# Kernel optimization log

Hardware: AMD Instinct MI355X
Metric: run time of the kernel (lower is better)

Reference implementation:

```python
import jax, jax.numpy as jnp
import numpy as np
from jax import lax

EPS = 1e-6
PPU = 256        # points_per_unit
MULT = 8         # 2 ** rho.num_halving_layers
C = 3            # in_channels (data channels)
NBASIS = 5
NS = 4           # num_samples
RHO_IN = 16      # encoder out / rho in channels
RHO_OUT = 32     # rho out channels
KW = 5           # conv kernel width


def setup_inputs() -> dict:
    key = jax.random.key(0)
    ks = jax.random.split(key, 16)
    nb, npts, ntar = 16, 2048, 256
    x = jax.random.uniform(ks[0], (nb, npts, C), jnp.float32)
    y = jax.random.normal(ks[1], (nb, npts, C), jnp.float32)
    x_out = jax.random.uniform(ks[2], (nb, ntar, C), jnp.float32)
    # --- compute_xgrid (done concretely at setup; mirrors torch logic) ---
    x_min = float(min(np.min(np.asarray(x)), np.min(np.asarray(x_out)))) - 0.1
    x_max = float(max(np.max(np.asarray(x)), np.max(np.asarray(x_out)))) + 0.1
    ngrid = int(np.ceil(PPU * (x_max - x_min) / MULT) * MULT)  # to_multiple
    grid = jnp.linspace(x_min, x_max, ngrid, dtype=jnp.float32)
    x_grid = jnp.broadcast_to(grid[None, :, None], (nb, ngrid, C))
    # --- parameters ---
    init_l = 2.0 / PPU
    enc_sigma = jnp.log(1e-6 + init_l * jnp.ones((C,), jnp.float32))
    int_sigma = jnp.log(1e-6 + init_l * jnp.ones((NBASIS, C), jnp.float32))
    s = 0.05
    gW = s * jax.random.normal(ks[3], (2 * C, RHO_IN), jnp.float32)
    gb = jnp.zeros((RHO_IN,), jnp.float32)
    w1 = s * jax.random.normal(ks[4], (RHO_OUT, RHO_IN, KW), jnp.float32)
    b1 = jnp.zeros((RHO_OUT,), jnp.float32)
    w2 = s * jax.random.normal(ks[5], (RHO_OUT, RHO_OUT, KW), jnp.float32)
    b2 = jnp.zeros((RHO_OUT,), jnp.float32)
    w3 = s * jax.random.normal(ks[6], (RHO_OUT, RHO_OUT, KW), jnp.float32)
    b3 = jnp.zeros((RHO_OUT,), jnp.float32)
    linW = s * jax.random.normal(ks[7], (RHO_OUT, 2 * C * NBASIS), jnp.float32)
    linb = jnp.zeros((2 * C * NBASIS,), jnp.float32)
    loW = s * jax.random.normal(ks[8], (C * NBASIS, 2 * C), jnp.float32)
    lob = jnp.zeros((2 * C,), jnp.float32)
    eps_noise = jax.random.normal(ks[9], (NS, nb, C * NBASIS), jnp.float32)
    return dict(x=x, y=y, x_out=x_out, x_grid=x_grid, eps_noise=eps_noise,
                enc_sigma=enc_sigma, gW=gW, gb=gb, w1=w1, b1=b1, w2=w2, b2=b2,
                w3=w3, b3=b3, linW=linW, linb=linb, int_sigma=int_sigma,
                loW=loW, lob=lob)


def _conv1d(h, w, b):
    # h: (N, Cin, L), w: (Cout, Cin, K) -> (N, Cout, L)
    return lax.conv_general_dilated(h, w, (1,), 'SAME',
                                    dimension_numbers=('NCH', 'OIH', 'NCH')) + b[None, :, None]


def reference(x, y, x_out, x_grid, eps_noise, enc_sigma, gW, gb,
              w1, b1, w2, b2, w3, b3, linW, linb, int_sigma, loW, lob):
    nb = x.shape[0]
    # ---- ConvDeepSet encoder: context points -> grid ----
    scales = jnp.exp(enc_sigma)                                  # (C,)
    d = (x[:, :, None, :] - x_grid[:, None, :, :]) / (scales + EPS)  # (nb,n,m,C)
    wt = jnp.exp(-0.5 * d * d)
    h0 = wt.sum(axis=1)                                          # (nb,m,C)
    h1 = (y[:, :, None, :] * wt).sum(axis=1)                     # (nb,m,C)
    n_h1 = h1 / (h0 + EPS)
    rep = jnp.concatenate([h0, n_h1], axis=-1) @ gW + gb         # (nb,m,RHO_IN)
    # ---- rho CNN on grid ----
    h = jax.nn.sigmoid(rep).transpose(0, 2, 1)                   # (nb,RHO_IN,m)
    h = jax.nn.relu(_conv1d(h, w1, b1))
    h = jax.nn.relu(_conv1d(h, w2, b2))
    h = _conv1d(h, w3, b3)                                       # (nb,RHO_OUT,m)
    h_grid = h.transpose(0, 2, 1) @ linW + linb                  # (nb,m,2*C*NBASIS)
    h_mu, h_std = jnp.split(h_grid, 2, axis=-1)
    h_std = 0.1 + 0.9 * jax.nn.sigmoid(h_std)
    # ---- latent samples ----
    z = h_mu[None] + h_std[None] * eps_noise[:, :, None, :]      # (NS,nb,m,C*NBASIS)
    ngrid = z.shape[2]
    z = z.reshape(NS * nb, ngrid, NBASIS, C)
    # ---- FinalLayer interpolator: grid -> targets ----
    xg = jnp.broadcast_to(x_grid[None], (NS,) + x_grid.shape).reshape(NS * nb, ngrid, C)
    xt = jnp.broadcast_to(x_out[None], (NS,) + x_out.shape).reshape(NS * nb, -1, C)
    iscales = jnp.exp(int_sigma)                                  # (NBASIS,C)
    dd = (xg[:, :, None, None, :] - xt[:, None, :, None, :]) / (iscales + EPS)
    wtt = jnp.exp(-0.5 * dd * dd)                                 # (NSnb,m,t,NBASIS,C)
    h_out = (z[:, :, None, :, :] * wtt).sum(axis=1)               # (NSnb,t,NBASIS,C)
    ntar = h_out.shape[1]
    out = h_out.reshape(NS * nb, ntar, NBASIS * C) @ loW + lob    # (NSnb,t,2C)
    mu, std = jnp.split(out, 2, axis=-1)
    std = jax.nn.softplus(std)
    return jnp.concatenate([mu, std], axis=-1).reshape(NS, nb, ntar, 2 * C)
```

## Files before the change

### kernel.cpp

```cpp
#include <hip/hip_runtime.h>
#include <math.h>

#define EPSF 1e-6f
#define LOG2E 1.4426950408889634f

__device__ __forceinline__ float sigmoidf_(float v) { return 1.0f / (1.0f + __expf(-v)); }

__global__ __launch_bounds__(512, 1) void encrho_kernel(
    const float* __restrict__ x, const float* __restrict__ y,
    const float* __restrict__ xg, const float* __restrict__ enc_sigma,
    const float* __restrict__ gW, const float* __restrict__ gb,
    const float* __restrict__ w1, const float* __restrict__ b1,
    const float* __restrict__ w2, const float* __restrict__ b2,
    const float* __restrict__ w3, const float* __restrict__ b3,
    const float* __restrict__ linW, const float* __restrict__ linb,
    float* __restrict__ mu, float* __restrict__ stdv,
    int nb, int M)
{
    __shared__ __align__(16) float smem[14856];
    float* sWA = smem;
    float* sWB = smem + 5152;
    float* sH1 = smem + 10304;
    float* sH2 = smem + 11200;
    float* sH3 = smem + 11968;
    float* sIn = smem + 12608;
    float* flt = smem;
    float* red = smem + 13120;
    float* tot = smem + 14656;
    float* sRange = smem + 14848;
    __shared__ int scnt[3];
    __shared__ int spad[3];

    const int tid = threadIdx.x;
    const int b = blockIdx.y;
    const int c0 = blockIdx.x * 20;
    const int ic = tid & 31, ng = tid >> 5;

    {
        float sg0 = __expf(enc_sigma[0]) + EPSF;
        float sg1 = __expf(enc_sigma[1]) + EPSF;
        float sg2 = __expf(enc_sigma[2]) + EPSF;
        float e20 = -0.5f * LOG2E / (sg0 * sg0);
        float e21 = -0.5f * LOG2E / (sg1 * sg1);
        float e22 = -0.5f * LOG2E / (sg2 * sg2);

        int mg = c0 - 6 + ic;
        bool cv = (mg >= 0 && mg < M);
        float g0 = 0, g1 = 0, g2 = 0;
        if (cv) {
            const float* gp = xg + (size_t)(b * M + mg) * 3;
            g0 = gp[0]; g1 = gp[1]; g2 = gp[2];
        }
        if (tid < 3) scnt[tid] = 0;
        if (tid < 96) {
            int c = tid >> 5;
            int col = c0 - 6 + ic;
            col = col < 0 ? 0 : (col >= M ? M - 1 : col);
            float gv = xg[(size_t)(b * M + col) * 3 + c];
            float gmn = gv, gmx = gv;
            #pragma unroll
            for (int mask = 1; mask <= 16; mask <<= 1) {
                gmn = fminf(gmn, __shfl_xor(gmn, mask, 64));
                gmx = fmaxf(gmx, __shfl_xor(gmx, mask, 64));
            }
            if (ic == 0) {
                float sgc = __expf(enc_sigma[c]) + EPSF;
                sRange[c] = gmn - 10.0f * sgc;
                sRange[3 + c] = gmx + 10.0f * sgc;
            }
        }
        __syncthreads();
        {
            const float* xb = x + (size_t)b * 6144;
            const float* yb = y + (size_t)b * 6144;
            #pragma unroll 1
            for (int idx = tid; idx < 6144; idx += 512) {
                float xv = xb[idx];
                int c = idx % 3;
                if (xv >= sRange[c] && xv <= sRange[3 + c]) {
                    int p = atomicAdd(&scnt[c], 1);
                    int o = (c << 12) + (p << 1);
                    flt[o] = xv;
                    flt[o + 1] = yb[idx];
                }
            }
        }
        __syncthreads();
        if (tid < 3) spad[tid] = (scnt[tid] + 31) & ~31;
        __syncthreads();
        #pragma unroll
        for (int c = 0; c < 3; c++) {
            int cnt = scnt[c], cp = spad[c];
            for (int p = cnt + tid; p < cp; p += 512) {
                int o = (c << 12) + (p << 1);
                flt[o] = 1e30f;
                flt[o + 1] = 0.0f;
            }
        }
        __syncthreads();
        float h[6];
        {
            const float2* f = (const float2*)flt;
            int cp = spad[0];
            float s0a = 0, s0b = 0, s1a = 0, s1b = 0;
            #pragma unroll 2
            for (int n = ng; n < cp; n += 32) {
                float2 va = f[n], vb = f[n + 16];
                float da = va.x - g0; float wa = exp2f(e20 * da * da);
                float db = vb.x - g0; float wb = exp2f(e20 * db * db);
                s0a += wa; s1a = fmaf(va.y, wa, s1a);
                s0b += wb; s1b = fmaf(vb.y, wb, s1b);
            }
            h[0] = s0a + s0b; h[3] = s1a + s1b;
        }
        {
            const float2* f = (const float2*)flt + 2048;
            int cp = spad[1];
            float s0a = 0, s0b = 0, s1a = 0, s1b = 0;
            #pragma unroll 2
            for (int n = ng; n < cp; n += 32) {
                float2 va = f[n], vb = f[n + 16];
                float da = va.x - g1; float wa = exp2f(e21 * da * da);
                float db = vb.x - g1; float wb = exp2f(e21 * db * db);
                s0a += wa; s1a = fmaf(va.y, wa, s1a);
                s0b += wb; s1b = fmaf(vb.y, wb, s1b);
            }
            h[1] = s0a + s0b; h[4] = s1a + s1b;
        }
        {
            const float2* f = (const float2*)flt + 4096;
            int cp = spad[2];
            float s0a = 0, s0b = 0, s1a = 0, s1b = 0;
            #pragma unroll 2
            for (int n = ng; n < cp; n += 32) {
                float2 va = f[n], vb = f[n + 16];
                float da = va.x - g2; float wa = exp2f(e22 * da * da);
                float db = vb.x - g2; float wb = exp2f(e22 * db * db);
                s0a += wa; s1a = fmaf(va.y, wa, s1a);
                s0b += wb; s1b = fmaf(vb.y, wb, s1b);
            }
            h[2] = s0a + s0b; h[5] = s1a + s1b;
        }
        __syncthreads();
        #pragma unroll
        for (int c = 0; c < 6; c++) h[c] += __shfl_xor(h[c], 32, 64);
        int lane = tid & 63, wv = tid >> 6;
        if (lane < 32) {
            float* rp = red + wv * 192 + lane * 6;
            #pragma unroll
            for (int c = 0; c < 6; c++) rp[c] = h[c];
        }
        {
            const float4* w1v4 = (const float4*)w1;
            const float4* w2v4 = (const float4*)w2;
            #pragma unroll 1
            for (int i4 = tid; i4 < 640; i4 += 512) {
                float4 v = w1v4[i4];
                float vv[4] = {v.x, v.y, v.z, v.w};
                #pragma unroll
                for (int j = 0; j < 4; j++) {
                    int e = 4 * i4 + j;
                    sWA[(e / 80) * 81 + e % 80] = vv[j];
                }
            }
            #pragma unroll 1
            for (int i4 = tid; i4 < 1280; i4 += 512) {
                float4 v = w2v4[i4];
                float vv[4] = {v.x, v.y, v.z, v.w};
                #pragma unroll
                for (int j = 0; j < 4; j++) {
                    int e = 4 * i4 + j;
                    sWB[(e / 160) * 161 + e % 160] = vv[j];
                }
            }
        }
        __syncthreads();
        if (tid < 192) {
            int ic2 = tid & 31, c = tid >> 5;
            float s = 0.0f;
            #pragma unroll
            for (int w = 0; w < 8; w++) s += red[w * 192 + ic2 * 6 + c];
            tot[ic2 * 6 + c] = s;
        }
        __syncthreads();
        {
            int j = tid >> 5, ic2 = tid & 31;
            int mg2 = c0 - 6 + ic2;
            float v = 0.0f;
            if (mg2 >= 0 && mg2 < M) {
                const float* tp = tot + ic2 * 6;
                float cat[6];
                #pragma unroll
                for (int c = 0; c < 3; c++) {
                    cat[c] = tp[c];
                    cat[3 + c] = tp[3 + c] / (tp[c] + EPSF);
                }
                float r = gb[j];
                #pragma unroll
                for (int i = 0; i < 6; i++) r = fmaf(cat[i], gW[i * 16 + j], r);
                v = sigmoidf_(r);
            }
            sIn[j * 32 + ic2] = v;
        }
    }
    __syncthreads();

    {
        int o = tid >> 4, q0 = tid & 15;
        {
            float a0 = b1[o], a1 = a0;
            bool two = (q0 < 12);
            #pragma unroll 2
            for (int i = 0; i < 16; i++) {
                const float* wp = sWA + o * 81 + i * 5;
                float u0 = wp[0], u1 = wp[1], u2 = wp[2], u3 = wp[3], u4 = wp[4];
                const float* ip = sIn + i * 32;
                a0 = fmaf(ip[q0], u0, a0);     a0 = fmaf(ip[q0+1], u1, a0);
                a0 = fmaf(ip[q0+2], u2, a0);   a0 = fmaf(ip[q0+3], u3, a0);
                a0 = fmaf(ip[q0+4], u4, a0);
                if (two) {
                    a1 = fmaf(ip[q0+16], u0, a1);  a1 = fmaf(ip[q0+17], u1, a1);
                    a1 = fmaf(ip[q0+18], u2, a1);  a1 = fmaf(ip[q0+19], u3, a1);
                    a1 = fmaf(ip[q0+20], u4, a1);
                }
            }
            int g0c = c0 - 4 + q0, g1c = g0c + 16;
            sH1[o * 28 + q0] = (g0c >= 0 && g0c < M) ? fmaxf(a0, 0.0f) : 0.0f;
            if (two) sH1[o * 28 + q0 + 16] = (g1c >= 0 && g1c < M) ? fmaxf(a1, 0.0f) : 0.0f;
        }
        __syncthreads();
        float4 wreg0, wreg1, wreg2;
        {
            const float4* w3v = (const float4*)w3;
            wreg0 = w3v[tid];
            wreg1 = w3v[tid + 512];
            if (tid < 256) wreg2 = w3v[tid + 1024];
        }
        {
            float a0 = b2[o], a1 = a0;
            bool two = (q0 < 8);
            #pragma unroll 2
            for (int i = 0; i < 32; i++) {
                const float* wp = sWB + o * 161 + i * 5;
                float u0 = wp[0], u1 = wp[1], u2 = wp[2], u3 = wp[3], u4 = wp[4];
                const float* ip = sH1 + i * 28;
                a0 = fmaf(ip[q0], u0, a0);     a0 = fmaf(ip[q0+1], u1, a0);
                a0 = fmaf(ip[q0+2], u2, a0);   a0 = fmaf(ip[q0+3], u3, a0);
                a0 = fmaf(ip[q0+4], u4, a0);
                if (two) {
                    a1 = fmaf(ip[q0+16], u0, a1);  a1 = fmaf(ip[q0+17], u1, a1);
                    a1 = fmaf(ip[q0+18], u2, a1);  a1 = fmaf(ip[q0+19], u3, a1);
                    a1 = fmaf(ip[q0+20], u4, a1);
                }
            }
            int g0c = c0 - 2 + q0, g1c = g0c + 16;
            sH2[o * 24 + q0] = (g0c >= 0 && g0c < M) ? fmaxf(a0, 0.0f) : 0.0f;
            if (two) sH2[o * 24 + q0 + 16] = (g1c >= 0 && g1c < M) ? fmaxf(a1, 0.0f) : 0.0f;
        }
        {
            float vv0[4] = {wreg0.x, wreg0.y, wreg0.z, wreg0.w};
            #pragma unroll
            for (int j = 0; j < 4; j++) {
                int e = 4 * tid + j;
                sWA[(e / 160) * 161 + e % 160] = vv0[j];
            }
            float vv1[4] = {wreg1.x, wreg1.y, wreg1.z, wreg1.w};
            #pragma unroll
            for (int j = 0; j < 4; j++) {
                int e = 4 * (tid + 512) + j;
                sWA[(e / 160) * 161 + e % 160] = vv1[j];
            }
            if (tid < 256) {
                float vv2[4] = {wreg2.x, wreg2.y, wreg2.z, wreg2.w};
                #pragma unroll
                for (int j = 0; j < 4; j++) {
                    int e = 4 * (tid + 1024) + j;
                    sWA[(e / 160) * 161 + e % 160] = vv2[j];
                }
            }
        }
        __syncthreads();
        {
            float a0 = b3[o], a1 = a0;
            bool two = (q0 < 4);
            #pragma unroll 2
            for (int i = 0; i < 32; i++) {
                const float* wp = sWA + o * 161 + i * 5;
                float u0 = wp[0], u1 = wp[1], u2 = wp[2], u3 = wp[3], u4 = wp[4];
                const float* ip = sH2 + i * 24;
                a0 = fmaf(ip[q0], u0, a0);     a0 = fmaf(ip[q0+1], u1, a0);
                a0 = fmaf(ip[q0+2], u2, a0);   a0 = fmaf(ip[q0+3], u3, a0);
                a0 = fmaf(ip[q0+4], u4, a0);
                if (two) {
                    a1 = fmaf(ip[q0+16], u0, a1);  a1 = fmaf(ip[q0+17], u1, a1);
                    a1 = fmaf(ip[q0+18], u2, a1);  a1 = fmaf(ip[q0+19], u3, a1);
                    a1 = fmaf(ip[q0+20], u4, a1);
                }
            }
            sH3[o * 20 + q0] = a0;
            if (two) sH3[o * 20 + q0 + 16] = a1;
        }
        __syncthreads();
        #pragma unroll 1
        for (int idx = tid; idx < 600; idx += 512) {
            int q = idx / 30, j = idx % 30;
            int m = c0 + q;
            if (m < M) {
                float v = linb[j];
                #pragma unroll 8
                for (int oo = 0; oo < 32; oo++) v = fmaf(sH3[oo * 20 + q], linW[oo * 30 + j], v);
                if (j < 15) mu[((size_t)b * M + m) * 16 + j] = v;
                else        stdv[((size_t)b * M + m) * 16 + (j - 15)] = 0.1f + 0.9f * sigmoidf_(v);
            }
        }
    }
}

__global__ __launch_bounds__(256, 4) void final_kernel(
    const float* __restrict__ x_out, const float* __restrict__ xg,
    const float* __restrict__ int_sigma, const float* __restrict__ eps,
    const float* __restrict__ mu, const float* __restrict__ stdv,
    const float* __restrict__ loW, const float* __restrict__ lob,
    float* __restrict__ out, int nb, int ntar, int M)
{
    __shared__ float red2[4][8][30];
    __shared__ float AB[8][30];
    int b = blockIdx.y;
    int tt = blockIdx.x * 8;
    int tid = threadIdx.x;
    int ti = tid & 7, mg = tid >> 3;
    int t = tt + ti;
    bool tv = (t < ntar);
    float xt[3];
    for (int c = 0; c < 3; c++) xt[c] = tv ? x_out[((size_t)b * ntar + t) * 3 + c] : 0.0f;
    float k2[15], Wc[3] = {0, 0, 0};
    #pragma unroll
    for (int k = 0; k < 15; k++) {
        float isc = __expf(int_sigma[k]) + EPSF;
        k2[k] = -0.5f * LOG2E / (isc * isc);
        Wc[k % 3] = fmaxf(Wc[k % 3], 10.0f * isc);
    }
    float gg0 = xg[(size_t)b * M * 3];
    float ggL = xg[((size_t)b * M + (M - 1)) * 3];
    float Dx = (ggL - gg0) / (float)(M - 1);
    float invDx = 1.0f / Dx;
    float A[15], B[15];
    #pragma unroll
    for (int k = 0; k < 15; k++) { A[k] = 0.0f; B[k] = 0.0f; }
    #pragma unroll
    for (int c = 0; c < 3; c++) {
        float xtc = xt[c];
        int lo = (int)floorf((xtc - Wc[c] - gg0) * invDx) - 1;
        int hi = (int)ceilf((xtc + Wc[c] - gg0) * invDx) + 1;
        lo = lo < 0 ? 0 : lo;
        hi = hi > M - 1 ? M - 1 : hi;
        #pragma unroll 1
        for (int m = lo + mg; m <= hi; m += 32) {
            float d = (gg0 + m * Dx) - xtc;
            float d2 = d * d;
            const float* mup = mu + ((size_t)b * M + m) * 16;
            const float* sdp = stdv + ((size_t)b * M + m) * 16;
            #pragma unroll
            for (int q = 0; q < 5; q++) {
                int k = c + 3 * q;
                float w = exp2f(k2[k] * d2);
                A[k] = fmaf(mup[k], w, A[k]);
                B[k] = fmaf(sdp[k], w, B[k]);
            }
        }
    }
    #pragma unroll
    for (int mask = 8; mask <= 32; mask <<= 1) {
        #pragma unroll
        for (int k = 0; k < 15; k++) {
            A[k] += __shfl_xor(A[k], mask, 64);
            B[k] += __shfl_xor(B[k], mask, 64);
        }
    }
    int lane = tid & 63, wv = tid >> 6;
    if (lane < 8) {
        #pragma unroll
        for (int k = 0; k < 15; k++) { red2[wv][lane][k] = A[k]; red2[wv][lane][15 + k] = B[k]; }
    }
    __syncthreads();
    if (tid < 240) {
        int t2 = tid / 30, v = tid % 30;
        AB[t2][v] = red2[0][t2][v] + red2[1][t2][v] + red2[2][t2][v] + red2[3][t2][v];
    }
    __syncthreads();
    if (tid < 192) {
        int t2 = tid / 24;
        int rem = tid % 24;
        int s = rem / 6, j = rem % 6;
        int tg = tt + t2;
        if (tg < ntar) {
            float val = lob[j];
            const float* ep = eps + ((size_t)s * nb + b) * 15;
            #pragma unroll
            for (int k = 0; k < 15; k++) {
                float h = fmaf(ep[k], AB[t2][15 + k], AB[t2][k]);
                val = fmaf(h, loW[k * 6 + j], val);
            }
            if (j >= 3) val = fmaxf(val, 0.0f) + log1pf(__expf(-fabsf(val)));
            out[(((size_t)s * nb + b) * ntar + tg) * 6 + j] = val;
        }
    }
}


__global__ __launch_bounds__(1024) void enc_kernel_g(
    const float* __restrict__ x, const float* __restrict__ y,
    const float* __restrict__ xg, const float* __restrict__ enc_sigma,
    const float* __restrict__ gW, const float* __restrict__ gb,
    float* __restrict__ rep_s, int nb, int npts, int M)
{
    __shared__ float sx[6144];
    __shared__ float sy[6144];
    __shared__ float red[16][8][6];
    __shared__ float tot[8][6];
    int b = blockIdx.y;
    int mt = blockIdx.x * 8;
    int tid = threadIdx.x;
    int n3 = npts * 3;
    if (n3 > 6144) n3 = 6144;
    for (int i = tid; i < n3; i += 1024) {
        sx[i] = x[(size_t)b * npts * 3 + i];
        sy[i] = y[(size_t)b * npts * 3 + i];
    }
    int npts_l = n3 / 3;
    int mi = tid & 7, ng = tid >> 3;
    int m = mt + mi;
    bool mv = (m < M);
    float e1[3], g[3];
    for (int c = 0; c < 3; c++) {
        float inv = 1.0f / (__expf(enc_sigma[c]) + EPSF);
        e1[c] = -0.5f * inv * inv;
    }
    for (int c = 0; c < 3; c++) g[c] = mv ? xg[(size_t)(b * M + m) * 3 + c] : 0.0f;
    __syncthreads();
    float h0[3] = {0,0,0}, h1[3] = {0,0,0};
    for (int n = ng; n < npts_l; n += 128) {
        for (int c = 0; c < 3; c++) {
            float d = sx[n * 3 + c] - g[c];
            float w = __expf(e1[c] * d * d);
            h0[c] += w;
            h1[c] = fmaf(sy[n * 3 + c], w, h1[c]);
        }
    }
    for (int mask = 8; mask <= 32; mask <<= 1) {
        for (int c = 0; c < 3; c++) {
            h0[c] += __shfl_xor(h0[c], mask, 64);
            h1[c] += __shfl_xor(h1[c], mask, 64);
        }
    }
    int lane = tid & 63, wv = tid >> 6;
    if (lane < 8) {
        for (int c = 0; c < 3; c++) { red[wv][lane][c] = h0[c]; red[wv][lane][3 + c] = h1[c]; }
    }
    __syncthreads();
    if (tid < 48) {
        int mi2 = tid & 7, c2 = tid >> 3;
        float s = 0.0f;
        for (int k = 0; k < 16; k++) s += red[k][mi2][c2];
        tot[mi2][c2] = s;
    }
    __syncthreads();
    if (tid < 128) {
        int mi2 = tid & 7, j = tid >> 3;
        int m2 = mt + mi2;
        if (m2 < M) {
            float cat[6];
            for (int c = 0; c < 3; c++) {
                cat[c] = tot[mi2][c];
                cat[3 + c] = tot[mi2][3 + c] / (tot[mi2][c] + EPSF);
            }
            float r = gb[j];
            for (int i = 0; i < 6; i++) r = fmaf(cat[i], gW[i * 16 + j], r);
            rep_s[((size_t)b * 16 + j) * M + m2] = sigmoidf_(r);
        }
    }
}

__global__ __launch_bounds__(256) void rho_kernel_g(
    const float* __restrict__ rep_s,
    const float* __restrict__ w1, const float* __restrict__ b1,
    const float* __restrict__ w2, const float* __restrict__ b2,
    const float* __restrict__ w3, const float* __restrict__ b3,
    const float* __restrict__ linW, const float* __restrict__ linb,
    float* __restrict__ mu, float* __restrict__ stdv,
    int nb, int M)
{
    __shared__ float sWA[5152];
    __shared__ float sWB[5152];
    __shared__ float sIn[16][20];
    __shared__ float sH1[32][16];
    __shared__ float sH2[32][12];
    __shared__ float sH3[32][8];
    int b = blockIdx.y;
    int t0 = blockIdx.x * 8;
    int tid = threadIdx.x;
    {
        const float4* w1v = (const float4*)w1;
        const float4* w2v = (const float4*)w2;
        for (int i4 = tid; i4 < 640; i4 += 256) {
            float4 v = w1v[i4];
            float vv[4] = {v.x, v.y, v.z, v.w};
            for (int j = 0; j < 4; j++) {
                int e = 4 * i4 + j;
                sWA[(e / 80) * 81 + e % 80] = vv[j];
            }
        }
        for (int i4 = tid; i4 < 1280; i4 += 256) {
            float4 v = w2v[i4];
            float vv[4] = {v.x, v.y, v.z, v.w};
            for (int j = 0; j < 4; j++) {
                int e = 4 * i4 + j;
                sWB[(e / 160) * 161 + e % 160] = vv[j];
            }
        }
        for (int idx = tid; idx < 16 * 20; idx += 256) {
            int i = idx / 20, q = idx % 20;
            int mg = t0 - 6 + q;
            sIn[i][q] = (mg >= 0 && mg < M) ? rep_s[((size_t)b * 16 + i) * M + mg] : 0.0f;
        }
    }
    __syncthreads();
    int o = tid >> 3, q0 = tid & 7;
    {
        float a0 = b1[o], a1 = a0;
        #pragma unroll 2
        for (int i = 0; i < 16; i++) {
            const float* wp = sWA + o * 81 + i * 5;
            float u0 = wp[0], u1 = wp[1], u2 = wp[2], u3 = wp[3], u4 = wp[4];
            const float* ip = &sIn[i][0];
            a0 = fmaf(ip[q0], u0, a0);      a0 = fmaf(ip[q0+1], u1, a0);
            a0 = fmaf(ip[q0+2], u2, a0);    a0 = fmaf(ip[q0+3], u3, a0);
            a0 = fmaf(ip[q0+4], u4, a0);
            a1 = fmaf(ip[q0+8], u0, a1);    a1 = fmaf(ip[q0+9], u1, a1);
            a1 = fmaf(ip[q0+10], u2, a1);   a1 = fmaf(ip[q0+11], u3, a1);
            a1 = fmaf(ip[q0+12], u4, a1);
        }
        int g0 = t0 - 4 + q0, g1 = g0 + 8;
        sH1[o][q0]     = (g0 >= 0 && g0 < M) ? fmaxf(a0, 0.0f) : 0.0f;
        sH1[o][q0 + 8] = (g1 >= 0 && g1 < M) ? fmaxf(a1, 0.0f) : 0.0f;
    }
    __syncthreads();
    float4 wreg[5];
    {
        const float4* w3v = (const float4*)w3;
        for (int h = 0; h < 5; h++) wreg[h] = w3v[tid + 256 * h];
    }
    {
        float a0 = b2[o], a1 = a0;
        bool second = (q0 < 4);
        #pragma unroll 2
        for (int i = 0; i < 32; i++) {
            const float* wp = sWB + o * 161 + i * 5;
            float u0 = wp[0], u1 = wp[1], u2 = wp[2], u3 = wp[3], u4 = wp[4];
            const float* ip = &sH1[i][0];
            a0 = fmaf(ip[q0], u0, a0);      a0 = fmaf(ip[q0+1], u1, a0);
            a0 = fmaf(ip[q0+2], u2, a0);    a0 = fmaf(ip[q0+3], u3, a0);
            a0 = fmaf(ip[q0+4], u4, a0);
            if (second) {
                a1 = fmaf(ip[q0+8], u0, a1);    a1 = fmaf(ip[q0+9], u1, a1);
                a1 = fmaf(ip[q0+10], u2, a1);   a1 = fmaf(ip[q0+11], u3, a1);
                a1 = fmaf(ip[q0+12], u4, a1);
            }
        }
        int g0 = t0 - 2 + q0, g1 = g0 + 8;
        sH2[o][q0] = (g0 >= 0 && g0 < M) ? fmaxf(a0, 0.0f) : 0.0f;
        if (second) sH2[o][q0 + 8] = (g1 >= 0 && g1 < M) ? fmaxf(a1, 0.0f) : 0.0f;
    }
    for (int h = 0; h < 5; h++) {
        float vv[4] = {wreg[h].x, wreg[h].y, wreg[h].z, wreg[h].w};
        for (int j = 0; j < 4; j++) {
            int e = 4 * (tid + 256 * h) + j;
            sWA[(e / 160) * 161 + e % 160] = vv[j];
        }
    }
    __syncthreads();
    {
        float a0 = b3[o];
        #pragma unroll 2
        for (int i = 0; i < 32; i++) {
            const float* wp = sWA + o * 161 + i * 5;
            float u0 = wp[0], u1 = wp[1], u2 = wp[2], u3 = wp[3], u4 = wp[4];
            const float* ip = &sH2[i][0];
            a0 = fmaf(ip[q0], u0, a0);      a0 = fmaf(ip[q0+1], u1, a0);
            a0 = fmaf(ip[q0+2], u2, a0);    a0 = fmaf(ip[q0+3], u3, a0);
            a0 = fmaf(ip[q0+4], u4, a0);
        }
        sH3[o][q0] = a0;
    }
    __syncthreads();
    if (tid < 240) {
        int q = tid / 30, j = tid % 30;
        int m = t0 + q;
        if (m < M) {
            float v = linb[j];
            #pragma unroll 8
            for (int oo = 0; oo < 32; oo++) v = fmaf(sH3[oo][q], linW[oo * 30 + j], v);
            if (j < 15) mu[((size_t)b * M + m) * 16 + j] = v;
            else        stdv[((size_t)b * M + m) * 16 + (j - 15)] = 0.1f + 0.9f * sigmoidf_(v);
        }
    }
}

extern "C" void kernel_launch(void* const* d_in, const int* in_sizes, int n_in,
                              void* d_out, int out_size, void* d_ws, size_t ws_size,
                              hipStream_t stream)
{
    const float* x         = (const float*)d_in[0];
    const float* y         = (const float*)d_in[1];
    const float* x_out     = (const float*)d_in[2];
    const float* x_grid    = (const float*)d_in[3];
    const float* eps_noise = (const float*)d_in[4];
    const float* enc_sigma = (const float*)d_in[5];
    const float* gW        = (const float*)d_in[6];
    const float* gb        = (const float*)d_in[7];
    const float* w1        = (const float*)d_in[8];
    const float* b1        = (const float*)d_in[9];
    const float* w2        = (const float*)d_in[10];
    const float* b2        = (const float*)d_in[11];
    const float* w3        = (const float*)d_in[12];
    const float* b3        = (const float*)d_in[13];
    const float* linW      = (const float*)d_in[14];
    const float* linb      = (const float*)d_in[15];
    const float* int_sigma = (const float*)d_in[16];
    const float* loW       = (const float*)d_in[17];
    const float* lob       = (const float*)d_in[18];
    float* out = (float*)d_out;

    const int NS = 4, C = 3, NBASIS = 5;
    int nb   = in_sizes[4] / (NS * C * NBASIS);
    int npts = in_sizes[0] / (nb * C);
    int ntar = in_sizes[2] / (nb * C);
    int M    = in_sizes[3] / (nb * C);

    float* mu   = (float*)d_ws;
    float* stdv = mu + (size_t)nb * M * 16;

    bool fast = (npts == 2048 && M <= 320);
    if (fast) {
        encrho_kernel<<<dim3(16, nb), 512, 0, stream>>>(
            x, y, x_grid, enc_sigma, gW, gb,
            w1, b1, w2, b2, w3, b3, linW, linb, mu, stdv, nb, M);
    } else {
        float* rep_s = stdv + (size_t)nb * M * 16;
        enc_kernel_g<<<dim3((M + 7) / 8, nb), 1024, 0, stream>>>(
            x, y, x_grid, enc_sigma, gW, gb, rep_s, nb, npts, M);
        rho_kernel_g<<<dim3((M + 7) / 8, nb), 256, 0, stream>>>(
            rep_s, w1, b1, w2, b2, w3, b3, linW, linb, mu, stdv, nb, M);
    }
    final_kernel<<<dim3((ntar + 7) / 8, nb), 256, 0, stream>>>(
        x_out, x_grid, int_sigma, eps_noise, mu, stdv, loW, lob, out, nb, ntar, M);
}
```

Before: 39.57 us.

## Transpose mu/std layout, ballot-based compaction, register-blocked convs, lane-contiguous final reduction

Moves the intermediate mu/std buffers to a channel-major layout so the final kernel's grid-point loop reads coalesced contiguous values. Thread mapping in the final kernel is changed so the 32 grid lanes for one target sit in a single wavefront, which removes the shared-memory cross-wave reduction. The encoder's point filtering now uses wave-level ballot plus one atomic per wave instead of one atomic per element. The three conv layers are reorganized so each thread computes 2 output channels by 2 positions from padded weight rows, using vector shared-memory loads. The cost is fewer active threads in the conv stages and a larger shared-memory footprint.

```diff
diff --git a/kernel.cpp b/kernel.cpp
--- a/kernel.cpp
+++ b/kernel.cpp
@@ -5,6 +5,17 @@
 #define LOG2E 1.4426950408889634f
 
 __device__ __forceinline__ float sigmoidf_(float v) { return 1.0f / (1.0f + __expf(-v)); }
+
+#define W1OFF   0
+#define W2OFF   4096
+#define W3OFF   0
+#define SINOFF  12288
+#define SH1OFF  12800
+#define SH2OFF  13696
+#define SH3TOFF 14464
+#define REDOFF  15104
+#define TOTOFF  16640
+#define RNGOFF  16832
 
 __global__ __launch_bounds__(512, 1) void encrho_kernel(
     const float* __restrict__ x, const float* __restrict__ y,
@@ -14,24 +25,16 @@
     const float* __restrict__ w2, const float* __restrict__ b2,
     const float* __restrict__ w3, const float* __restrict__ b3,
     const float* __restrict__ linW, const float* __restrict__ linb,
-    float* __restrict__ mu, float* __restrict__ stdv,
+    float* __restrict__ mu_t, float* __restrict__ stdv_t,
     int nb, int M)
 {
-    __shared__ __align__(16) float smem[14856];
-    float* sWA = smem;
-    float* sWB = smem + 5152;
-    float* sH1 = smem + 10304;
-    float* sH2 = smem + 11200;
-    float* sH3 = smem + 11968;
-    float* sIn = smem + 12608;
-    float* flt = smem;
-    float* red = smem + 13120;
-    float* tot = smem + 14656;
-    float* sRange = smem + 14848;
+    __shared__ __align__(16) float smem[16840];
     __shared__ int scnt[3];
     __shared__ int spad[3];
+    float* flt = smem;
 
     const int tid = threadIdx.x;
+    const int lane = tid & 63;
     const int b = blockIdx.y;
     const int c0 = blockIdx.x * 20;
     const int ic = tid & 31, ng = tid >> 5;
@@ -65,23 +68,32 @@
             }
             if (ic == 0) {
                 float sgc = __expf(enc_sigma[c]) + EPSF;
-                sRange[c] = gmn - 10.0f * sgc;
-                sRange[3 + c] = gmx + 10.0f * sgc;
+                smem[RNGOFF + c] = gmn - 10.0f * sgc;
+                smem[RNGOFF + 3 + c] = gmx + 10.0f * sgc;
             }
         }
         __syncthreads();
         {
             const float* xb = x + (size_t)b * 6144;
             const float* yb = y + (size_t)b * 6144;
-            #pragma unroll 1
-            for (int idx = tid; idx < 6144; idx += 512) {
+            for (int base = 0; base < 6144; base += 512) {
+                int idx = base + tid;
                 float xv = xb[idx];
+                float yv = yb[idx];
                 int c = idx % 3;
-                if (xv >= sRange[c] && xv <= sRange[3 + c]) {
-                    int p = atomicAdd(&scnt[c], 1);
-                    int o = (c << 12) + (p << 1);
-                    flt[o] = xv;
-                    flt[o + 1] = yb[idx];
+                bool pass = (xv >= smem[RNGOFF + c] && xv <= smem[RNGOFF + 3 + c]);
+                #pragma unroll
+                for (int t = 0; t < 3; t++) {
+                    unsigned long long mball = __ballot(pass && (c == t));
+                    int bpos = 0;
+                    if (lane == 0) bpos = atomicAdd(&scnt[t], __popcll(mball));
+                    bpos = __shfl(bpos, 0, 64);
+                    if (pass && (c == t)) {
+                        int pos = bpos + __popcll(mball & ((1ull << lane) - 1ull));
+                        int o = (t << 12) + (pos << 1);
+                        flt[o] = xv;
+                        flt[o + 1] = yv;
+                    }
                 }
             }
         }
@@ -144,9 +156,9 @@
         __syncthreads();
         #pragma unroll
         for (int c = 0; c < 6; c++) h[c] += __shfl_xor(h[c], 32, 64);
-        int lane = tid & 63, wv = tid >> 6;
+        int wv = tid >> 6;
         if (lane < 32) {
-            float* rp = red + wv * 192 + lane * 6;
+            float* rp = smem + REDOFF + wv * 192 + lane * 6;
             #pragma unroll
             for (int c = 0; c < 6; c++) rp[c] = h[c];
         }
@@ -160,7 +172,8 @@
                 #pragma unroll
                 for (int j = 0; j < 4; j++) {
                     int e = 4 * i4 + j;
-                    sWA[(e / 80) * 81 + e % 80] = vv[j];
+                    int row = e / 5;
+                    smem[W1OFF + row * 8 + (e - row * 5)] = vv[j];
                 }
             }
             #pragma unroll 1
@@ -170,7 +183,8 @@
                 #pragma unroll
                 for (int j = 0; j < 4; j++) {
                     int e = 4 * i4 + j;
-                    sWB[(e / 160) * 161 + e % 160] = vv[j];
+                    int row = e / 5;
+                    smem[W2OFF + row * 8 + (e - row * 5)] = vv[j];
                 }
             }
         }
@@ -179,8 +193,8 @@
             int ic2 = tid & 31, c = tid >> 5;
             float s = 0.0f;
             #pragma unroll
-            for (int w = 0; w < 8; w++) s += red[w * 192 + ic2 * 6 + c];
-            tot[ic2 * 6 + c] = s;
+            for (int w = 0; w < 8; w++) s += smem[REDOFF + w * 192 + ic2 * 6 + c];
+            smem[TOTOFF + ic2 * 6 + c] = s;
         }
         __syncthreads();
         {
@@ -188,7 +202,7 @@
             int mg2 = c0 - 6 + ic2;
             float v = 0.0f;
             if (mg2 >= 0 && mg2 < M) {
-                const float* tp = tot + ic2 * 6;
+                const float* tp = smem + TOTOFF + ic2 * 6;
                 float cat[6];
                 #pragma unroll
                 for (int c = 0; c < 3; c++) {
@@ -200,33 +214,47 @@
                 for (int i = 0; i < 6; i++) r = fmaf(cat[i], gW[i * 16 + j], r);
                 v = sigmoidf_(r);
             }
-            sIn[j * 32 + ic2] = v;
+            smem[SINOFF + j * 32 + ic2] = v;
         }
     }
     __syncthreads();
 
     {
-        int o = tid >> 4, q0 = tid & 15;
-        {
-            float a0 = b1[o], a1 = a0;
-            bool two = (q0 < 12);
+        if (tid < 224) {
+            int o2 = tid / 14, cg = tid - o2 * 14;
+            int oA = o2 * 2, oB = oA + 1;
+            float aA0 = b1[oA], aA1 = aA0;
+            float aB0 = b1[oB], aB1 = aB0;
             #pragma unroll 2
             for (int i = 0; i < 16; i++) {
-                const float* wp = sWA + o * 81 + i * 5;
-                float u0 = wp[0], u1 = wp[1], u2 = wp[2], u3 = wp[3], u4 = wp[4];
-                const float* ip = sIn + i * 32;
-                a0 = fmaf(ip[q0], u0, a0);     a0 = fmaf(ip[q0+1], u1, a0);
-                a0 = fmaf(ip[q0+2], u2, a0);   a0 = fmaf(ip[q0+3], u3, a0);
-                a0 = fmaf(ip[q0+4], u4, a0);
-                if (two) {
-                    a1 = fmaf(ip[q0+16], u0, a1);  a1 = fmaf(ip[q0+17], u1, a1);
-                    a1 = fmaf(ip[q0+18], u2, a1);  a1 = fmaf(ip[q0+19], u3, a1);
-                    a1 = fmaf(ip[q0+20], u4, a1);
-                }
-            }
-            int g0c = c0 - 4 + q0, g1c = g0c + 16;
-            sH1[o * 28 + q0] = (g0c >= 0 && g0c < M) ? fmaxf(a0, 0.0f) : 0.0f;
-            if (two) sH1[o * 28 + q0 + 16] = (g1c >= 0 && g1c < M) ? fmaxf(a1, 0.0f) : 0.0f;
+                const float* ip = smem + SINOFF + i * 32 + 2 * cg;
+                float2 f01 = *(const float2*)ip;
+                float2 f23 = *(const float2*)(ip + 2);
+                float2 f45 = *(const float2*)(ip + 4);
+                const float* wA = smem + W1OFF + (oA * 16 + i) * 8;
+                const float* wB = smem + W1OFF + (oB * 16 + i) * 8;
+                float4 wa = *(const float4*)wA; float wa4 = wA[4];
+                float4 wb = *(const float4*)wB; float wb4 = wB[4];
+                aA0 = fmaf(f01.x, wa.x, aA0); aA0 = fmaf(f01.y, wa.y, aA0);
+                aA0 = fmaf(f23.x, wa.z, aA0); aA0 = fmaf(f23.y, wa.w, aA0);
+                aA0 = fmaf(f45.x, wa4, aA0);
+                aA1 = fmaf(f01.y, wa.x, aA1); aA1 = fmaf(f23.x, wa.y, aA1);
+                aA1 = fmaf(f23.y, wa.z, aA1); aA1 = fmaf(f45.x, wa.w, aA1);
+                aA1 = fmaf(f45.y, wa4, aA1);
+                aB0 = fmaf(f01.x, wb.x, aB0); aB0 = fmaf(f01.y, wb.y, aB0);
+                aB0 = fmaf(f23.x, wb.z, aB0); aB0 = fmaf(f23.y, wb.w, aB0);
+                aB0 = fmaf(f45.x, wb4, aB0);
+                aB1 = fmaf(f01.y, wb.x, aB1); aB1 = fmaf(f23.x, wb.y, aB1);
+                aB1 = fmaf(f23.y, wb.z, aB1); aB1 = fmaf(f45.x, wb.w, aB1);
+                aB1 = fmaf(f45.y, wb4, aB1);
+            }
+            int q = 2 * cg;
+            int gq = c0 - 4 + q;
+            bool v0 = (gq >= 0 && gq < M), v1 = (gq + 1 >= 0 && gq + 1 < M);
+            smem[SH1OFF + oA * 28 + q]     = v0 ? fmaxf(aA0, 0.f) : 0.f;
+            smem[SH1OFF + oA * 28 + q + 1] = v1 ? fmaxf(aA1, 0.f) : 0.f;
+            smem[SH1OFF + oB * 28 + q]     = v0 ? fmaxf(aB0, 0.f) : 0.f;
+            smem[SH1OFF + oB * 28 + q + 1] = v1 ? fmaxf(aB1, 0.f) : 0.f;
         }
         __syncthreads();
         float4 wreg0, wreg1, wreg2;
@@ -236,81 +264,121 @@
             wreg1 = w3v[tid + 512];
             if (tid < 256) wreg2 = w3v[tid + 1024];
         }
-        {
-            float a0 = b2[o], a1 = a0;
-            bool two = (q0 < 8);
+        if (tid < 192) {
+            int o2 = tid / 12, cg = tid - o2 * 12;
+            int oA = o2 * 2, oB = oA + 1;
+            float aA0 = b2[oA], aA1 = aA0;
+            float aB0 = b2[oB], aB1 = aB0;
             #pragma unroll 2
             for (int i = 0; i < 32; i++) {
-                const float* wp = sWB + o * 161 + i * 5;
-                float u0 = wp[0], u1 = wp[1], u2 = wp[2], u3 = wp[3], u4 = wp[4];
-                const float* ip = sH1 + i * 28;
-                a0 = fmaf(ip[q0], u0, a0);     a0 = fmaf(ip[q0+1], u1, a0);
-                a0 = fmaf(ip[q0+2], u2, a0);   a0 = fmaf(ip[q0+3], u3, a0);
-                a0 = fmaf(ip[q0+4], u4, a0);
-                if (two) {
-                    a1 = fmaf(ip[q0+16], u0, a1);  a1 = fmaf(ip[q0+17], u1, a1);
-                    a1 = fmaf(ip[q0+18], u2, a1);  a1 = fmaf(ip[q0+19], u3, a1);
-                    a1 = fmaf(ip[q0+20], u4, a1);
-                }
-            }
-            int g0c = c0 - 2 + q0, g1c = g0c + 16;
-            sH2[o * 24 + q0] = (g0c >= 0 && g0c < M) ? fmaxf(a0, 0.0f) : 0.0f;
-            if (two) sH2[o * 24 + q0 + 16] = (g1c >= 0 && g1c < M) ? fmaxf(a1, 0.0f) : 0.0f;
+                const float* ip = smem + SH1OFF + i * 28 + 2 * cg;
+                float2 f01 = *(const float2*)ip;
+                float2 f23 = *(const float2*)(ip + 2);
+                float2 f45 = *(const float2*)(ip + 4);
+                const float* wA = smem + W2OFF + (oA * 32 + i) * 8;
+                const float* wB = smem + W2OFF + (oB * 32 + i) * 8;
+                float4 wa = *(const float4*)wA; float wa4 = wA[4];
+                float4 wb = *(const float4*)wB; float wb4 = wB[4];
+                aA0 = fmaf(f01.x, wa.x, aA0); aA0 = fmaf(f01.y, wa.y, aA0);
+                aA0 = fmaf(f23.x, wa.z, aA0); aA0 = fmaf(f23.y, wa.w, aA0);
+                aA0 = fmaf(f45.x, wa4, aA0);
+                aA1 = fmaf(f01.y, wa.x, aA1); aA1 = fmaf(f23.x, wa.y, aA1);
+                aA1 = fmaf(f23.y, wa.z, aA1); aA1 = fmaf(f45.x, wa.w, aA1);
+                aA1 = fmaf(f45.y, wa4, aA1);
+                aB0 = fmaf(f01.x, wb.x, aB0); aB0 = fmaf(f01.y, wb.y, aB0);
+                aB0 = fmaf(f23.x, wb.z, aB0); aB0 = fmaf(f23.y, wb.w, aB0);
+                aB0 = fmaf(f45.x, wb4, aB0);
+                aB1 = fmaf(f01.y, wb.x, aB1); aB1 = fmaf(f23.x, wb.y, aB1);
+                aB1 = fmaf(f23.y, wb.z, aB1); aB1 = fmaf(f45.x, wb.w, aB1);
+                aB1 = fmaf(f45.y, wb4, aB1);
+            }
+            int q = 2 * cg;
+            int gq = c0 - 2 + q;
+            bool v0 = (gq >= 0 && gq < M), v1 = (gq + 1 >= 0 && gq + 1 < M);
+            smem[SH2OFF + oA * 24 + q]     = v0 ? fmaxf(aA0, 0.f) : 0.f;
+            smem[SH2OFF + oA * 24 + q + 1] = v1 ? fmaxf(aA1, 0.f) : 0.f;
+            smem[SH2OFF + oB * 24 + q]     = v0 ? fmaxf(aB0, 0.f) : 0.f;
+            smem[SH2OFF + oB * 24 + q + 1] = v1 ? fmaxf(aB1, 0.f) : 0.f;
         }
         {
             float vv0[4] = {wreg0.x, wreg0.y, wreg0.z, wreg0.w};
             #pragma unroll
             for (int j = 0; j < 4; j++) {
                 int e = 4 * tid + j;
-                sWA[(e / 160) * 161 + e % 160] = vv0[j];
+                int row = e / 5;
+                smem[W3OFF + row * 8 + (e - row * 5)] = vv0[j];
             }
             float vv1[4] = {wreg1.x, wreg1.y, wreg1.z, wreg1.w};
             #pragma unroll
             for (int j = 0; j < 4; j++) {
                 int e = 4 * (tid + 512) + j;
-                sWA[(e / 160) * 161 + e % 160] = vv1[j];
+                int row = e / 5;
+                smem[W3OFF + row * 8 + (e - row * 5)] = vv1[j];
             }
             if (tid < 256) {
                 float vv2[4] = {wreg2.x, wreg2.y, wreg2.z, wreg2.w};
                 #pragma unroll
                 for (int j = 0; j < 4; j++) {
                     int e = 4 * (tid + 1024) + j;
-                    sWA[(e / 160) * 161 + e % 160] = vv2[j];
+                    int row = e / 5;
+                    smem[W3OFF + row * 8 + (e - row * 5)] = vv2[j];
                 }
             }
         }
         __syncthreads();
-        {
-            float a0 = b3[o], a1 = a0;
-            bool two = (q0 < 4);
+        if (tid < 160) {
+            int o2 = tid / 10, cg = tid - o2 * 10;
+            int oA = o2 * 2, oB = oA + 1;
+            float aA0 = b3[oA], aA1 = aA0;
+            float aB0 = b3[oB], aB1 = aB0;
             #pragma unroll 2
             for (int i = 0; i < 32; i++) {
-                const float* wp = sWA + o * 161 + i * 5;
-                float u0 = wp[0], u1 = wp[1], u2 = wp[2], u3 = wp[3], u4 = wp[4];
-                const float* ip = sH2 + i * 24;
-                a0 = fmaf(ip[q0], u0, a0);     a0 = fmaf(ip[q0+1], u1, a0);
-                a0 = fmaf(ip[q0+2], u2, a0);   a0 = fmaf(ip[q0+3], u3, a0);
-                a0 = fmaf(ip[q0+4], u4, a0);
-                if (two) {
-                    a1 = fmaf(ip[q0+16], u0, a1);  a1 = fmaf(ip[q0+17], u1, a1);
-                    a1 = fmaf(ip[q0+18], u2, a1);  a1 = fmaf(ip[q0+19], u3, a1);
-                    a1 = fmaf(ip[q0+20], u4, a1);
-                }
-            }
-            sH3[o * 20 + q0] = a0;
-            if (two) sH3[o * 20 + q0 + 16] = a1;
+                const float* ip = smem + SH2OFF + i * 24 + 2 * cg;
+                float2 f01 = *(const float2*)ip;
+                float2 f23 = *(const float2*)(ip + 2);
+                float2 f45 = *(const float2*)(ip + 4);
+                const float* wA = smem + W3OFF + (oA * 32 + i) * 8;
+                const float* wB = smem + W3OFF + (oB * 32 + i) * 8;
+                float4 wa = *(const float4*)wA; float wa4 = wA[4];
+                float4 wb = *(const float4*)wB; float wb4 = wB[4];
+                aA0 = fmaf(f01.x, wa.x, aA0); aA0 = fmaf(f01.y, wa.y, aA0);
+                aA0 = fmaf(f23.x, wa.z, aA0); aA0 = fmaf(f23.y, wa.w, aA0);
+                aA0 = fmaf(f45.x, wa4, aA0);
+                aA1 = fmaf(f01.y, wa.x, aA1); aA1 = fmaf(f23.x, wa.y, aA1);
+                aA1 = fmaf(f23.y, wa.z, aA1); aA1 = fmaf(f45.x, wa.w, aA1);
+                aA1 = fmaf(f45.y, wa4, aA1);
+                aB0 = fmaf(f01.x, wb.x, aB0); aB0 = fmaf(f01.y, wb.y, aB0);
+                aB0 = fmaf(f23.x, wb.z, aB0); aB0 = fmaf(f23.y, wb.w, aB0);
+                aB0 = fmaf(f45.x, wb4, aB0);
+                aB1 = fmaf(f01.y, wb.x, aB1); aB1 = fmaf(f23.x, wb.y, aB1);
+                aB1 = fmaf(f23.y, wb.z, aB1); aB1 = fmaf(f45.x, wb.w, aB1);
+                aB1 = fmaf(f45.y, wb4, aB1);
+            }
+            int q = 2 * cg;
+            smem[SH3TOFF + q * 32 + oA]       = aA0;
+            smem[SH3TOFF + (q + 1) * 32 + oA] = aA1;
+            smem[SH3TOFF + q * 32 + oB]       = aB0;
+            smem[SH3TOFF + (q + 1) * 32 + oB] = aB1;
         }
         __syncthreads();
         #pragma unroll 1
         for (int idx = tid; idx < 600; idx += 512) {
-            int q = idx / 30, j = idx % 30;
+            int q = idx / 30, j = idx - (idx / 30) * 30;
             int m = c0 + q;
             if (m < M) {
+                const float* hp = smem + SH3TOFF + q * 32;
                 float v = linb[j];
-                #pragma unroll 8
-                for (int oo = 0; oo < 32; oo++) v = fmaf(sH3[oo * 20 + q], linW[oo * 30 + j], v);
-                if (j < 15) mu[((size_t)b * M + m) * 16 + j] = v;
-                else        stdv[((size_t)b * M + m) * 16 + (j - 15)] = 0.1f + 0.9f * sigmoidf_(v);
+                #pragma unroll
+                for (int o4 = 0; o4 < 8; o4++) {
+                    float4 h4 = *(const float4*)(hp + o4 * 4);
+                    const float* lw = linW + o4 * 4 * 30 + j;
+                    v = fmaf(h4.x, lw[0], v);
+                    v = fmaf(h4.y, lw[30], v);
+                    v = fmaf(h4.z, lw[60], v);
+                    v = fmaf(h4.w, lw[90], v);
+                }
+                if (j < 15) mu_t[((size_t)b * 15 + j) * M + m] = v;
+                else        stdv_t[((size_t)b * 15 + (j - 15)) * M + m] = 0.1f + 0.9f * sigmoidf_(v);
             }
         }
     }
@@ -319,19 +387,19 @@
 __global__ __launch_bounds__(256, 4) void final_kernel(
     const float* __restrict__ x_out, const float* __restrict__ xg,
     const float* __restrict__ int_sigma, const float* __restrict__ eps,
-    const float* __restrict__ mu, const float* __restrict__ stdv,
+    const float* __restrict__ mu_t, const float* __restrict__ stdv_t,
     const float* __restrict__ loW, const float* __restrict__ lob,
     float* __restrict__ out, int nb, int ntar, int M)
 {
-    __shared__ float red2[4][8][30];
     __shared__ float AB[8][30];
     int b = blockIdx.y;
     int tt = blockIdx.x * 8;
     int tid = threadIdx.x;
-    int ti = tid & 7, mg = tid >> 3;
+    int mg = tid & 31, ti = tid >> 5;
     int t = tt + ti;
     bool tv = (t < ntar);
     float xt[3];
+    #pragma unroll
     for (int c = 0; c < 3; c++) xt[c] = tv ? x_out[((size_t)b * ntar + t) * 3 + c] : 0.0f;
     float k2[15], Wc[3] = {0, 0, 0};
     #pragma unroll
@@ -354,44 +422,49 @@
         int hi = (int)ceilf((xtc + Wc[c] - gg0) * invDx) + 1;
         lo = lo < 0 ? 0 : lo;
         hi = hi > M - 1 ? M - 1 : hi;
+        const float* pm0 = mu_t + ((size_t)b * 15 + c) * M;
+        const float* pm1 = pm0 + 3 * M;
+        const float* pm2 = pm0 + 6 * M;
+        const float* pm3 = pm0 + 9 * M;
+        const float* pm4 = pm0 + 12 * M;
+        const float* ps0 = stdv_t + ((size_t)b * 15 + c) * M;
+        const float* ps1 = ps0 + 3 * M;
+        const float* ps2 = ps0 + 6 * M;
+        const float* ps3 = ps0 + 9 * M;
+        const float* ps4 = ps0 + 12 * M;
         #pragma unroll 1
         for (int m = lo + mg; m <= hi; m += 32) {
             float d = (gg0 + m * Dx) - xtc;
             float d2 = d * d;
-            const float* mup = mu + ((size_t)b * M + m) * 16;
-            const float* sdp = stdv + ((size_t)b * M + m) * 16;
-            #pragma unroll
-            for (int q = 0; q < 5; q++) {
-                int k = c + 3 * q;
-                float w = exp2f(k2[k] * d2);
-                A[k] = fmaf(mup[k], w, A[k]);
-                B[k] = fmaf(sdp[k], w, B[k]);
-            }
+            float w0 = exp2f(k2[c] * d2);
+            float w1v = exp2f(k2[c + 3] * d2);
+            float w2v = exp2f(k2[c + 6] * d2);
+            float w3v = exp2f(k2[c + 9] * d2);
+            float w4v = exp2f(k2[c + 12] * d2);
+            A[c]      = fmaf(pm0[m], w0, A[c]);       B[c]      = fmaf(ps0[m], w0, B[c]);
+            A[c + 3]  = fmaf(pm1[m], w1v, A[c + 3]);  B[c + 3]  = fmaf(ps1[m], w1v, B[c + 3]);
+            A[c + 6]  = fmaf(pm2[m], w2v, A[c + 6]);  B[c + 6]  = fmaf(ps2[m], w2v, B[c + 6]);
+            A[c + 9]  = fmaf(pm3[m], w3v, A[c + 9]);  B[c + 9]  = fmaf(ps3[m], w3v, B[c + 9]);
+            A[c + 12] = fmaf(pm4[m], w4v, A[c + 12]); B[c + 12] = fmaf(ps4[m], w4v, B[c + 12]);
         }
     }
     #pragma unroll
-    for (int mask = 8; mask <= 32; mask <<= 1) {
+    for (int mask = 1; mask <= 16; mask <<= 1) {
         #pragma unroll
         for (int k = 0; k < 15; k++) {
             A[k] += __shfl_xor(A[k], mask, 64);
             B[k] += __shfl_xor(B[k], mask, 64);
         }
     }
-    int lane = tid & 63, wv = tid >> 6;
-    if (lane < 8) {
+    if (mg == 0) {
         #pragma unroll
-        for (int k = 0; k < 15; k++) { red2[wv][lane][k] = A[k]; red2[wv][lane][15 + k] = B[k]; }
-    }
-    __syncthreads();
-    if (tid < 240) {
-        int t2 = tid / 30, v = tid % 30;
-        AB[t2][v] = red2[0][t2][v] + red2[1][t2][v] + red2[2][t2][v] + red2[3][t2][v];
+        for (int k = 0; k < 15; k++) { AB[ti][k] = A[k]; AB[ti][15 + k] = B[k]; }
     }
     __syncthreads();
     if (tid < 192) {
         int t2 = tid / 24;
-        int rem = tid % 24;
-        int s = rem / 6, j = rem % 6;
+        int rem = tid - t2 * 24;
+        int s = rem / 6, j = rem - s * 6;
         int tg = tt + t2;
         if (tg < ntar) {
             float val = lob[j];
@@ -487,7 +560,7 @@
     const float* __restrict__ w2, const float* __restrict__ b2,
     const float* __restrict__ w3, const float* __restrict__ b3,
     const float* __restrict__ linW, const float* __restrict__ linb,
-    float* __restrict__ mu, float* __restrict__ stdv,
+    float* __restrict__ mu_t, float* __restrict__ stdv_t,
     int nb, int M)
 {
     __shared__ float sWA[5152];
@@ -600,8 +673,8 @@
             float v = linb[j];
             #pragma unroll 8
             for (int oo = 0; oo < 32; oo++) v = fmaf(sH3[oo][q], linW[oo * 30 + j], v);
-            if (j < 15) mu[((size_t)b * M + m) * 16 + j] = v;
-            else        stdv[((size_t)b * M + m) * 16 + (j - 15)] = 0.1f + 0.9f * sigmoidf_(v);
+            if (j < 15) mu_t[((size_t)b * 15 + j) * M + m] = v;
+            else        stdv_t[((size_t)b * 15 + (j - 15)) * M + m] = 0.1f + 0.9f * sigmoidf_(v);
         }
     }
 }
@@ -637,21 +710,21 @@
     int ntar = in_sizes[2] / (nb * C);
     int M    = in_sizes[3] / (nb * C);
 
-    float* mu   = (float*)d_ws;
-    float* stdv = mu + (size_t)nb * M * 16;
+    float* mu_t   = (float*)d_ws;
+    float* stdv_t = mu_t + (size_t)nb * 15 * M;
 
     bool fast = (npts == 2048 && M <= 320);
     if (fast) {
         encrho_kernel<<<dim3(16, nb), 512, 0, stream>>>(
             x, y, x_grid, enc_sigma, gW, gb,
-            w1, b1, w2, b2, w3, b3, linW, linb, mu, stdv, nb, M);
+            w1, b1, w2, b2, w3, b3, linW, linb, mu_t, stdv_t, nb, M);
     } else {
-        float* rep_s = stdv + (size_t)nb * M * 16;
+        float* rep_s = stdv_t + (size_t)nb * 15 * M;
         enc_kernel_g<<<dim3((M + 7) / 8, nb), 1024, 0, stream>>>(
             x, y, x_grid, enc_sigma, gW, gb, rep_s, nb, npts, M);
         rho_kernel_g<<<dim3((M + 7) / 8, nb), 256, 0, stream>>>(
-            rep_s, w1, b1, w2, b2, w3, b3, linW, linb, mu, stdv, nb, M);
+            rep_s, w1, b1, w2, b2, w3, b3, linW, linb, mu_t, stdv_t, nb, M);
     }
     final_kernel<<<dim3((ntar + 7) / 8, nb), 256, 0, stream>>>(
-        x_out, x_grid, int_sigma, eps_noise, mu, stdv, loW, lob, out, nb, ntar, M);
+        x_out, x_grid, int_sigma, eps_noise, mu_t, stdv_t, loW, lob, out, nb, ntar, M);
 }
```

Measured after the change: 41.65 us. 1.05x slower.
